# Performance work log

Hardware: AMD Instinct MI355X
Metric: run time of the kernel (lower is better)

The kernel has to match this reference:

```python
import jax, jax.numpy as jnp
import numpy as np

K_EXPERTS = 2  # init kwarg k_experts

def _glu_mlp(x, up_w, gate_w, down_w):
    # gated MLP: down( up(x) * GELU(gate(x)) ), exact-erf GELU matching torch nn.GELU()
    h = (x @ up_w) * jax.nn.gelu(x @ gate_w, approximate=False)
    return h @ down_w

def setup_inputs() -> dict:
    key = jax.random.key(0)
    ks = jax.random.split(key, 8)
    B, S, D, I, E = 2, 2048, 1024, 512, 8
    sc = 0.02
    return {
        "x": jax.random.normal(ks[0], (B, S, D), jnp.float32),
        "gate_w": jax.random.normal(ks[1], (E, D), jnp.float32) * sc,
        "up_w": jax.random.normal(ks[2], (E, D, I), jnp.float32) * sc,
        "gproj_w": jax.random.normal(ks[3], (E, D, I), jnp.float32) * sc,
        "down_w": jax.random.normal(ks[4], (E, I, D), jnp.float32) * sc,
        "shared_up_w": jax.random.normal(ks[5], (D, I), jnp.float32) * sc,
        "shared_gate_w": jax.random.normal(ks[6], (D, I), jnp.float32) * sc,
        "shared_down_w": jax.random.normal(ks[7], (I, D), jnp.float32) * sc,
    }

def reference(x, gate_w, up_w, gproj_w, down_w, shared_up_w, shared_gate_w, shared_down_w):
    B, S, D = x.shape
    E = gate_w.shape[0]
    xf = x.reshape(-1, D)                      # [T, D]
    T = xf.shape[0]

    # --- SigmaGate: softmax over expert logits, top-k, renormalize ---
    logits = xf @ gate_w.T                     # [T, E]
    scores = jax.nn.softmax(logits, axis=-1)
    topk_w, topk_idx = jax.lax.top_k(scores, K_EXPERTS)   # [T, k]
    topk_w = topk_w / (topk_w.sum(axis=-1, keepdims=True) + 1e-20)

    # combine weights as dense [T, E] (topk indices are distinct per token)
    combine = jnp.zeros((T, E), xf.dtype).at[jnp.arange(T)[:, None], topk_idx].add(topk_w)

    # --- experts: scan over E, accumulate weighted expert outputs ---
    def step(acc, ws):
        uw, gw, dw, ce = ws                    # ce: [T] combine weight for this expert
        y_e = _glu_mlp(xf, uw, gw, dw)         # [T, D]
        return acc + ce[:, None] * y_e, None

    y, _ = jax.lax.scan(step, jnp.zeros_like(xf), (up_w, gproj_w, down_w, combine.T))

    # --- shared expert on identity ---
    y = y + _glu_mlp(xf, shared_up_w, shared_gate_w, shared_down_w)
    return y.reshape(B, S, D)
```

## Files before the change

### kernel.cpp

```cpp
#include <hip/hip_runtime.h>
#include <hip/hip_bf16.h>
#include <math.h>

#define T_TOK 4096
#define D_DIM 1024
#define I_DIM 512
#define E_EXP 8
#define KSEL 2
#define NPAIR (T_TOK * KSEL)
#define ROUTED_CAP 9216
#define SHARED_BASE ROUTED_CAP
#define RTOT (ROUTED_CAP + T_TOK)
#define MAXTILES 104
#define GRID_G (MAXTILES * 8)

typedef __bf16 bf16x8 __attribute__((ext_vector_type(8)));
typedef float f32x4 __attribute__((ext_vector_type(4)));
typedef unsigned short ushort8 __attribute__((ext_vector_type(8)));

constexpr size_t SZ_XB  = (size_t)T_TOK * D_DIM * 2;
constexpr size_t SZ_UG  = (size_t)E_EXP * 2 * I_DIM * D_DIM * 2;
constexpr size_t SZ_DT  = (size_t)E_EXP * I_DIM * D_DIM * 2;
constexpr size_t SZ_SUG = (size_t)2 * I_DIM * D_DIM * 2;
constexpr size_t SZ_SDT = (size_t)I_DIM * D_DIM * 2;
constexpr size_t SZ_H   = (size_t)RTOT * I_DIM * 2;
constexpr size_t SZ_Y   = (size_t)RTOT * D_DIM * 2;

constexpr size_t OFF_XB   = 0;
constexpr size_t OFF_UG   = OFF_XB  + SZ_XB;
constexpr size_t OFF_DT   = OFF_UG  + SZ_UG;
constexpr size_t OFF_SUG  = OFF_DT  + SZ_DT;
constexpr size_t OFF_SDT  = OFF_SUG + SZ_SUG;
constexpr size_t OFF_H    = OFF_SDT + SZ_SDT;
constexpr size_t OFF_Y    = OFF_H   + SZ_H;
constexpr size_t OFF_TOPKI= OFF_Y   + SZ_Y;
constexpr size_t OFF_TOPKW= OFF_TOPKI + (size_t)NPAIR * 4;
constexpr size_t OFF_INV  = OFF_TOPKW + (size_t)NPAIR * 4;
constexpr size_t OFF_PERM = OFF_INV   + (size_t)NPAIR * 4;
constexpr size_t OFF_META = OFF_PERM  + (size_t)RTOT * 4;

__device__ __forceinline__ unsigned short f2bf(float f) {
  unsigned int u = __float_as_uint(f);
  unsigned int r = (u + 0x7FFFu + ((u >> 16) & 1u)) >> 16;
  return (unsigned short)r;
}
__device__ __forceinline__ float bf2f(unsigned short s) {
  return __uint_as_float(((unsigned int)s) << 16);
}
__device__ __forceinline__ void gload_lds16(const void* g, void* l) {
  __builtin_amdgcn_global_load_lds(
      (const __attribute__((address_space(1))) void*)g,
      (__attribute__((address_space(3))) void*)l, 16, 0, 0);
}

__global__ void transpose_cvt_all(
    const float* __restrict__ upw, const float* __restrict__ gpw,
    const float* __restrict__ dww, const float* __restrict__ sup,
    const float* __restrict__ sgt, const float* __restrict__ sdw,
    unsigned short* __restrict__ UG, unsigned short* __restrict__ sUG,
    unsigned short* __restrict__ Dt, unsigned short* __restrict__ sDt) {
  __shared__ float t[32][33];
  int bid = blockIdx.x;
  const float* in; unsigned short* out;
  int R, C, xt, yt, mode;
  if (bid < 4096)       { int e = bid >> 9, s = bid & 511;
    in = upw + (size_t)e * D_DIM * I_DIM; out = UG + (size_t)e * 2 * I_DIM * D_DIM;
    R = D_DIM; C = I_DIM; xt = s & 15; yt = s >> 4; mode = 0; }
  else if (bid < 8192)  { int b = bid - 4096; int e = b >> 9, s = b & 511;
    in = gpw + (size_t)e * D_DIM * I_DIM; out = UG + (size_t)e * 2 * I_DIM * D_DIM;
    R = D_DIM; C = I_DIM; xt = s & 15; yt = s >> 4; mode = 1; }
  else if (bid < 12288) { int b = bid - 8192; int e = b >> 9, s = b & 511;
    in = dww + (size_t)e * I_DIM * D_DIM; out = Dt + (size_t)e * I_DIM * D_DIM;
    R = I_DIM; C = D_DIM; xt = s & 31; yt = s >> 5; mode = 2; }
  else if (bid < 12800) { int s = bid - 12288;
    in = sup; out = sUG; R = D_DIM; C = I_DIM; xt = s & 15; yt = s >> 4; mode = 0; }
  else if (bid < 13312) { int s = bid - 12800;
    in = sgt; out = sUG; R = D_DIM; C = I_DIM; xt = s & 15; yt = s >> 4; mode = 1; }
  else                  { int s = bid - 13312;
    in = sdw; out = sDt; R = I_DIM; C = D_DIM; xt = s & 31; yt = s >> 5; mode = 2; }
  int c0 = xt * 32, r0 = yt * 32;
  int tx = threadIdx.x, ty = threadIdx.y;
#pragma unroll
  for (int i = 0; i < 4; ++i)
    t[ty + 8 * i][tx] = in[(size_t)(r0 + ty + 8 * i) * C + c0 + tx];
  __syncthreads();
#pragma unroll
  for (int i = 0; i < 4; ++i) {
    int c = c0 + ty + 8 * i;
    int orow = (mode == 2) ? c : (((c >> 4) << 5) + (c & 15) + (mode == 1 ? 16 : 0));
    out[(size_t)orow * R + r0 + tx] = f2bf(t[tx][ty + 8 * i]);
  }
}

__global__ void gating_kernel(const float* __restrict__ x, const float* __restrict__ gw,
                              unsigned short* __restrict__ xb,
                              int* __restrict__ topk_idx, float* __restrict__ topk_w) {
  int lane = threadIdx.x & 63;
  int t = blockIdx.x * 4 + (threadIdx.x >> 6);
  const float4* xr = (const float4*)(x + (size_t)t * D_DIM);
  float4 xv[4];
#pragma unroll
  for (int j = 0; j < 4; ++j) xv[j] = xr[lane + 64 * j];
#pragma unroll
  for (int j = 0; j < 4; ++j) {
    ushort4 o;
    o.x = f2bf(xv[j].x); o.y = f2bf(xv[j].y); o.z = f2bf(xv[j].z); o.w = f2bf(xv[j].w);
    *(ushort4*)&xb[(size_t)t * D_DIM + (lane + 64 * j) * 4] = o;
  }
  float acc[E_EXP];
#pragma unroll
  for (int e = 0; e < E_EXP; ++e) {
    const float4* gr = (const float4*)(gw + (size_t)e * D_DIM);
    float a = 0.f;
#pragma unroll
    for (int j = 0; j < 4; ++j) {
      float4 g = gr[lane + 64 * j];
      a += xv[j].x * g.x + xv[j].y * g.y + xv[j].z * g.z + xv[j].w * g.w;
    }
    acc[e] = a;
  }
#pragma unroll
  for (int off = 32; off; off >>= 1)
#pragma unroll
    for (int e = 0; e < E_EXP; ++e) acc[e] += __shfl_xor(acc[e], off, 64);
  if (lane == 0) {
    int i0 = 0; float m0 = acc[0];
#pragma unroll
    for (int e = 1; e < E_EXP; ++e) if (acc[e] > m0) { m0 = acc[e]; i0 = e; }
    int i1 = -1; float m1 = -1e30f;
#pragma unroll
    for (int e = 0; e < E_EXP; ++e) if (e != i0 && acc[e] > m1) { m1 = acc[e]; i1 = e; }
    float e1 = __expf(m1 - m0);
    float w0 = 1.0f / (1.0f + e1);
    float w1 = e1 / (1.0f + e1);
    topk_idx[2 * t] = i0; topk_idx[2 * t + 1] = i1;
    topk_w[2 * t] = w0;   topk_w[2 * t + 1] = w1;
  }
}

__global__ __launch_bounds__(1024) void route_kernel(
    const int* __restrict__ tidx, int* __restrict__ meta,
    int* __restrict__ perm, int* __restrict__ inv) {
  __shared__ int els[NPAIR];
  __shared__ int cnt_iw[128][E_EXP];
  __shared__ int base_iw[128][E_EXP];
  __shared__ int ebase[E_EXP];
  __shared__ int ecnt[E_EXP];
  int tid = threadIdx.x, lane = tid & 63, wv = tid >> 6;

  for (int it = 0; it < NPAIR / 1024; ++it) {
    int g = it * 1024 + tid;
    int e = tidx[g];
    els[g] = e;
#pragma unroll
    for (int ex = 0; ex < E_EXP; ++ex) {
      unsigned long long m = __ballot(e == ex);
      if (lane == 0) cnt_iw[it * 16 + wv][ex] = __popcll(m);
    }
  }
  __syncthreads();

  if (tid < E_EXP) {
    int s = 0;
    for (int iw = 0; iw < 128; ++iw) { base_iw[iw][tid] = s; s += cnt_iw[iw][tid]; }
    ecnt[tid] = s;
  }
  __syncthreads();

  if (tid == 0) {
    int o = 0, tc = 0;
    int2* m2 = (int2*)meta;
    for (int e = 0; e < E_EXP; ++e) {
      ebase[e] = o;
      int c = ecnt[e];
      int pt = (c + 127) >> 7;
      for (int ti = 0; ti < pt; ++ti) m2[tc++] = make_int2(e, o + ti * 128);
      o += pt * 128;
    }
    for (int ti = 0; ti < T_TOK / 128; ++ti)
      m2[tc++] = make_int2(E_EXP, SHARED_BASE + ti * 128);
    for (; tc < MAXTILES; ++tc) m2[tc] = make_int2(-1, 0);
  }
  __syncthreads();

  for (int it = 0; it < NPAIR / 1024; ++it) {
    int g = it * 1024 + tid;
    int e = els[g];
    int rank = 0;
#pragma unroll
    for (int ex = 0; ex < E_EXP; ++ex) {
      unsigned long long m = __ballot(e == ex);
      if (e == ex) rank = __popcll(m & ((1ull << lane) - 1ull));
    }
    int row = ebase[e] + base_iw[it * 16 + wv][e] + rank;
    perm[row] = g >> 1;
    inv[g] = row;
  }
  {
    int p = tid;
    int e = p >> 7, s = p & 127;
    int c = ecnt[e];
    int padn = (((c + 127) >> 7) << 7) - c;
    if (s < padn) perm[ebase[e] + c + s] = 0;
  }
  for (int t = tid; t < T_TOK; t += 1024) perm[SHARED_BASE + t] = t;
}

__global__ __launch_bounds__(256, 2) void gemm1_kernel(
    const unsigned short* __restrict__ xb, const unsigned short* __restrict__ UG,
    const unsigned short* __restrict__ sUG, unsigned short* __restrict__ H,
    const int* __restrict__ meta, const int* __restrict__ perm) {
  int orig = blockIdx.x;
  int wg = (orig & 7) * (GRID_G / 8) + (orig >> 3);
  int mt = wg >> 3, nt = wg & 7;
  int2 m2 = ((const int2*)meta)[mt];
  int e = m2.x;
  if (e < 0) return;
  int base = m2.y;
  int n0 = nt * 128;
  const unsigned short* B = (e < E_EXP) ? UG + (size_t)e * 2 * I_DIM * D_DIM : sUG;

  __shared__ unsigned short As[2 * 128 * 64];
  __shared__ unsigned short Bs[2 * 128 * 64];

  int tid = threadIdx.x, lane = tid & 63, wv = tid >> 6;
  const unsigned short *gA[4], *gB[4];
  int dL[4];
#pragma unroll
  for (int j = 0; j < 4; ++j) {
    int c = j * 256 + tid;
    int row = c >> 3, q = c & 7, qs = q ^ (row & 7);
    int tok = perm[base + row];
    gA[j] = xb + (size_t)tok * D_DIM + qs * 8;
    gB[j] = B + (size_t)(n0 + row) * D_DIM + qs * 8;
    dL[j] = (j * 256 + wv * 64) * 8;
  }

  f32x4 acc[4][4] = {};
  int wr = (wv >> 1) * 64, wc = (wv & 1) * 64;
  int l15 = lane & 15, l4 = lane >> 4;
  int sx = l15 & 7;

#define STAGE1(buf, k0) do { \
  _Pragma("unroll") \
  for (int j = 0; j < 4; ++j) { \
    gload_lds16(gA[j] + (k0), As + (buf) * 8192 + dL[j]); \
    gload_lds16(gB[j] + (k0), Bs + (buf) * 8192 + dL[j]); \
  } } while (0)

  STAGE1(0, 0);
  const int NK = D_DIM / 64;
  for (int t = 0; t < NK; ++t) {
    int cur = t & 1;
    if (t + 1 < NK) {
      STAGE1(cur ^ 1, (t + 1) * 64);
      asm volatile("s_waitcnt vmcnt(8)" ::: "memory");
    } else {
      asm volatile("s_waitcnt vmcnt(0)" ::: "memory");
    }
    __builtin_amdgcn_s_barrier();
    bf16x8 af[2][4], bfr[2][4];
#pragma unroll
    for (int kh = 0; kh < 2; ++kh) {
      int kb = kh * 4 + l4;
#pragma unroll
      for (int i = 0; i < 4; ++i) {
        af[kh][i]  = *reinterpret_cast<const bf16x8*>(&As[cur * 8192 + (wr + i * 16 + l15) * 64 + (kb ^ sx) * 8]);
        bfr[kh][i] = *reinterpret_cast<const bf16x8*>(&Bs[cur * 8192 + (wc + i * 16 + l15) * 64 + (kb ^ sx) * 8]);
      }
    }
    asm volatile("" ::: "memory");
    __builtin_amdgcn_s_barrier();
    __builtin_amdgcn_s_setprio(1);
#pragma unroll
    for (int kh = 0; kh < 2; ++kh)
#pragma unroll
      for (int i = 0; i < 4; ++i)
#pragma unroll
        for (int j = 0; j < 4; ++j)
          acc[i][j] = __builtin_amdgcn_mfma_f32_16x16x32_bf16(af[kh][i], bfr[kh][j], acc[i][j], 0, 0, 0);
    __builtin_amdgcn_s_setprio(0);
  }
#undef STAGE1

  const float is2 = 0.70710678118654752f;
  int hbase = (n0 >> 1) + (wv & 1) * 32;
#pragma unroll
  for (int i = 0; i < 4; ++i) {
    int row = base + wr + i * 16 + l4 * 4;
#pragma unroll
    for (int m = 0; m < 2; ++m) {
      int col = hbase + m * 16 + l15;
#pragma unroll
      for (int r = 0; r < 4; ++r) {
        float u = acc[i][2 * m][r], g = acc[i][2 * m + 1][r];
        float gl = 0.5f * g * (1.0f + erff(g * is2));
        H[(size_t)(row + r) * I_DIM + col] = f2bf(u * gl);
      }
    }
  }
}

__global__ __launch_bounds__(256, 2) void gemm2_kernel(
    const unsigned short* __restrict__ H, const unsigned short* __restrict__ Dt,
    const unsigned short* __restrict__ sDt, unsigned short* __restrict__ Y,
    const int* __restrict__ meta) {
  int orig = blockIdx.x;
  int wg = (orig & 7) * (GRID_G / 8) + (orig >> 3);
  int mt = wg >> 3, nt = wg & 7;
  int2 m2 = ((const int2*)meta)[mt];
  int e = m2.x;
  if (e < 0) return;
  int base = m2.y;
  int n0 = nt * 128;
  const unsigned short* B = (e < E_EXP) ? Dt + (size_t)e * D_DIM * I_DIM : sDt;

  __shared__ unsigned short As[2 * 128 * 64];
  __shared__ unsigned short Bs[2 * 128 * 64];

  int tid = threadIdx.x, lane = tid & 63, wv = tid >> 6;
  const unsigned short *gA[4], *gB[4];
  int dL[4];
#pragma unroll
  for (int j = 0; j < 4; ++j) {
    int c = j * 256 + tid;
    int row = c >> 3, q = c & 7, qs = q ^ (row & 7);
    gA[j] = H + (size_t)(base + row) * I_DIM + qs * 8;
    gB[j] = B + (size_t)(n0 + row) * I_DIM + qs * 8;
    dL[j] = (j * 256 + wv * 64) * 8;
  }

  f32x4 acc[4][4] = {};
  int wr = (wv >> 1) * 64, wc = (wv & 1) * 64;
  int l15 = lane & 15, l4 = lane >> 4;
  int sx = l15 & 7;

#define STAGE2(buf, k0) do { \
  _Pragma("unroll") \
  for (int j = 0; j < 4; ++j) { \
    gload_lds16(gA[j] + (k0), As + (buf) * 8192 + dL[j]); \
    gload_lds16(gB[j] + (k0), Bs + (buf) * 8192 + dL[j]); \
  } } while (0)

  STAGE2(0, 0);
  const int NK = I_DIM / 64;
  for (int t = 0; t < NK; ++t) {
    int cur = t & 1;
    if (t + 1 < NK) {
      STAGE2(cur ^ 1, (t + 1) * 64);
      asm volatile("s_waitcnt vmcnt(8)" ::: "memory");
    } else {
      asm volatile("s_waitcnt vmcnt(0)" ::: "memory");
    }
    __builtin_amdgcn_s_barrier();
    bf16x8 af[2][4], bfr[2][4];
#pragma unroll
    for (int kh = 0; kh < 2; ++kh) {
      int kb = kh * 4 + l4;
#pragma unroll
      for (int i = 0; i < 4; ++i) {
        af[kh][i]  = *reinterpret_cast<const bf16x8*>(&As[cur * 8192 + (wr + i * 16 + l15) * 64 + (kb ^ sx) * 8]);
        bfr[kh][i] = *reinterpret_cast<const bf16x8*>(&Bs[cur * 8192 + (wc + i * 16 + l15) * 64 + (kb ^ sx) * 8]);
      }
    }
    asm volatile("" ::: "memory");
    __builtin_amdgcn_s_barrier();
    __builtin_amdgcn_s_setprio(1);
#pragma unroll
    for (int kh = 0; kh < 2; ++kh)
#pragma unroll
      for (int i = 0; i < 4; ++i)
#pragma unroll
        for (int j = 0; j < 4; ++j)
          acc[i][j] = __builtin_amdgcn_mfma_f32_16x16x32_bf16(af[kh][i], bfr[kh][j], acc[i][j], 0, 0, 0);
    __builtin_amdgcn_s_setprio(0);
  }
#undef STAGE2

#pragma unroll
  for (int i = 0; i < 4; ++i) {
    int row = base + wr + i * 16 + l4 * 4;
#pragma unroll
    for (int j = 0; j < 4; ++j) {
      int col = n0 + wc + j * 16 + l15;
#pragma unroll
      for (int r = 0; r < 4; ++r)
        Y[(size_t)(row + r) * D_DIM + col] = f2bf(acc[i][j][r]);
    }
  }
}

__global__ void combine_kernel(const unsigned short* __restrict__ Y, const int* __restrict__ inv,
                               const float* __restrict__ tw, float* __restrict__ out) {
  int g = blockIdx.x * 256 + threadIdx.x;
  int t = g >> 7, d0 = (g & 127) * 8;
  int r0 = inv[2 * t], r1 = inv[2 * t + 1];
  float w0 = tw[2 * t], w1 = tw[2 * t + 1];
  ushort8 y0 = *(const ushort8*)&Y[(size_t)r0 * D_DIM + d0];
  ushort8 y1 = *(const ushort8*)&Y[(size_t)r1 * D_DIM + d0];
  ushort8 ys = *(const ushort8*)&Y[(size_t)(SHARED_BASE + t) * D_DIM + d0];
  float o[8];
#pragma unroll
  for (int j = 0; j < 8; ++j)
    o[j] = w0 * bf2f(y0[j]) + w1 * bf2f(y1[j]) + bf2f(ys[j]);
  float4* op = (float4*)(out + (size_t)t * D_DIM + d0);
  op[0] = make_float4(o[0], o[1], o[2], o[3]);
  op[1] = make_float4(o[4], o[5], o[6], o[7]);
}

extern "C" void kernel_launch(void* const* d_in, const int* in_sizes, int n_in,
                              void* d_out, int out_size, void* d_ws, size_t ws_size,
                              hipStream_t stream) {
  const float* x    = (const float*)d_in[0];
  const float* gw   = (const float*)d_in[1];
  const float* upw  = (const float*)d_in[2];
  const float* gpw  = (const float*)d_in[3];
  const float* dww  = (const float*)d_in[4];
  const float* sup  = (const float*)d_in[5];
  const float* sgt  = (const float*)d_in[6];
  const float* sdw  = (const float*)d_in[7];
  float* out = (float*)d_out;

  char* ws = (char*)d_ws;
  unsigned short* xb  = (unsigned short*)(ws + OFF_XB);
  unsigned short* UG  = (unsigned short*)(ws + OFF_UG);
  unsigned short* Dt  = (unsigned short*)(ws + OFF_DT);
  unsigned short* sUG = (unsigned short*)(ws + OFF_SUG);
  unsigned short* sDt = (unsigned short*)(ws + OFF_SDT);
  unsigned short* H   = (unsigned short*)(ws + OFF_H);
  unsigned short* Y   = (unsigned short*)(ws + OFF_Y);
  int*   tki   = (int*)(ws + OFF_TOPKI);
  float* tkw   = (float*)(ws + OFF_TOPKW);
  int*   inv   = (int*)(ws + OFF_INV);
  int*   perm  = (int*)(ws + OFF_PERM);
  int*   meta  = (int*)(ws + OFF_META);

  transpose_cvt_all<<<13824, dim3(32, 8), 0, stream>>>(upw, gpw, dww, sup, sgt, sdw,
                                                       UG, sUG, Dt, sDt);
  gating_kernel<<<T_TOK / 4, 256, 0, stream>>>(x, gw, xb, tki, tkw);
  route_kernel<<<1, 1024, 0, stream>>>(tki, meta, perm, inv);

  gemm1_kernel<<<GRID_G, 256, 0, stream>>>(xb, UG, sUG, H, meta, perm);
  gemm2_kernel<<<GRID_G, 256, 0, stream>>>(H, Dt, sDt, Y, meta);
  combine_kernel<<<(T_TOK * 128) / 256, 256, 0, stream>>>(Y, inv, tkw, out);
}
```

Measured before the change: 110.5 us.

## Enlarge MoE GEMM tiles to 256x256 with 512-thread blocks

Both grouped GEMM kernels move from 128x128 tiles with 4 waves to 256x256 tiles with 8 waves, each wave computing a 128x64 sub-tile. Routing pads expert segments to 256 rows, so the routed capacity and tile metadata change to match. The LDS fragment loads are interleaved per k-half with the MFMAs to keep register pressure in check. Larger tiles raise arithmetic intensity and cut how often weights are re-read. In exchange there are fewer workgroups (224 vs 832) to fill the CUs, more padding rows per expert, double the LDS per block, and higher register use.

```diff
diff --git a/kernel.cpp b/kernel.cpp
--- a/kernel.cpp
+++ b/kernel.cpp
@@ -8,11 +8,11 @@
 #define E_EXP 8
 #define KSEL 2
 #define NPAIR (T_TOK * KSEL)
-#define ROUTED_CAP 9216
+#define ROUTED_CAP 10240
 #define SHARED_BASE ROUTED_CAP
 #define RTOT (ROUTED_CAP + T_TOK)
-#define MAXTILES 104
-#define GRID_G (MAXTILES * 8)
+#define MAXTILES 56
+#define GRID_G (MAXTILES * 4)
 
 typedef __bf16 bf16x8 __attribute__((ext_vector_type(8)));
 typedef float f32x4 __attribute__((ext_vector_type(4)));
@@ -173,12 +173,12 @@
     for (int e = 0; e < E_EXP; ++e) {
       ebase[e] = o;
       int c = ecnt[e];
-      int pt = (c + 127) >> 7;
-      for (int ti = 0; ti < pt; ++ti) m2[tc++] = make_int2(e, o + ti * 128);
-      o += pt * 128;
-    }
-    for (int ti = 0; ti < T_TOK / 128; ++ti)
-      m2[tc++] = make_int2(E_EXP, SHARED_BASE + ti * 128);
+      int pt = (c + 255) >> 8;
+      for (int ti = 0; ti < pt; ++ti) m2[tc++] = make_int2(e, o + ti * 256);
+      o += pt * 256;
+    }
+    for (int ti = 0; ti < T_TOK / 256; ++ti)
+      m2[tc++] = make_int2(E_EXP, SHARED_BASE + ti * 256);
     for (; tc < MAXTILES; ++tc) m2[tc] = make_int2(-1, 0);
   }
   __syncthreads();
@@ -196,56 +196,55 @@
     perm[row] = g >> 1;
     inv[g] = row;
   }
-  {
-    int p = tid;
-    int e = p >> 7, s = p & 127;
+  for (int p = tid; p < E_EXP * 256; p += 1024) {
+    int e = p >> 8, s = p & 255;
     int c = ecnt[e];
-    int padn = (((c + 127) >> 7) << 7) - c;
+    int padn = (((c + 255) >> 8) << 8) - c;
     if (s < padn) perm[ebase[e] + c + s] = 0;
   }
   for (int t = tid; t < T_TOK; t += 1024) perm[SHARED_BASE + t] = t;
 }
 
-__global__ __launch_bounds__(256, 2) void gemm1_kernel(
+__global__ __launch_bounds__(512, 2) void gemm1_kernel(
     const unsigned short* __restrict__ xb, const unsigned short* __restrict__ UG,
     const unsigned short* __restrict__ sUG, unsigned short* __restrict__ H,
     const int* __restrict__ meta, const int* __restrict__ perm) {
   int orig = blockIdx.x;
   int wg = (orig & 7) * (GRID_G / 8) + (orig >> 3);
-  int mt = wg >> 3, nt = wg & 7;
+  int mt = wg >> 2, nt = wg & 3;
   int2 m2 = ((const int2*)meta)[mt];
   int e = m2.x;
   if (e < 0) return;
   int base = m2.y;
-  int n0 = nt * 128;
+  int n0 = nt * 256;
   const unsigned short* B = (e < E_EXP) ? UG + (size_t)e * 2 * I_DIM * D_DIM : sUG;
 
-  __shared__ unsigned short As[2 * 128 * 64];
-  __shared__ unsigned short Bs[2 * 128 * 64];
+  __shared__ unsigned short As[2 * 256 * 64];
+  __shared__ unsigned short Bs[2 * 256 * 64];
 
   int tid = threadIdx.x, lane = tid & 63, wv = tid >> 6;
   const unsigned short *gA[4], *gB[4];
   int dL[4];
 #pragma unroll
   for (int j = 0; j < 4; ++j) {
-    int c = j * 256 + tid;
+    int c = j * 512 + tid;
     int row = c >> 3, q = c & 7, qs = q ^ (row & 7);
     int tok = perm[base + row];
     gA[j] = xb + (size_t)tok * D_DIM + qs * 8;
     gB[j] = B + (size_t)(n0 + row) * D_DIM + qs * 8;
-    dL[j] = (j * 256 + wv * 64) * 8;
-  }
-
-  f32x4 acc[4][4] = {};
-  int wr = (wv >> 1) * 64, wc = (wv & 1) * 64;
+    dL[j] = (j * 512 + wv * 64) * 8;
+  }
+
+  f32x4 acc[8][4] = {};
+  int wr = (wv >> 2) * 128, wc = (wv & 3) * 64;
   int l15 = lane & 15, l4 = lane >> 4;
   int sx = l15 & 7;
 
 #define STAGE1(buf, k0) do { \
   _Pragma("unroll") \
   for (int j = 0; j < 4; ++j) { \
-    gload_lds16(gA[j] + (k0), As + (buf) * 8192 + dL[j]); \
-    gload_lds16(gB[j] + (k0), Bs + (buf) * 8192 + dL[j]); \
+    gload_lds16(gA[j] + (k0), As + (buf) * 16384 + dL[j]); \
+    gload_lds16(gB[j] + (k0), Bs + (buf) * 16384 + dL[j]); \
   } } while (0)
 
   STAGE1(0, 0);
@@ -259,41 +258,40 @@
       asm volatile("s_waitcnt vmcnt(0)" ::: "memory");
     }
     __builtin_amdgcn_s_barrier();
-    bf16x8 af[2][4], bfr[2][4];
 #pragma unroll
     for (int kh = 0; kh < 2; ++kh) {
       int kb = kh * 4 + l4;
-#pragma unroll
-      for (int i = 0; i < 4; ++i) {
-        af[kh][i]  = *reinterpret_cast<const bf16x8*>(&As[cur * 8192 + (wr + i * 16 + l15) * 64 + (kb ^ sx) * 8]);
-        bfr[kh][i] = *reinterpret_cast<const bf16x8*>(&Bs[cur * 8192 + (wc + i * 16 + l15) * 64 + (kb ^ sx) * 8]);
-      }
+      bf16x8 af[8], bfr[4];
+#pragma unroll
+      for (int i = 0; i < 8; ++i)
+        af[i] = *reinterpret_cast<const bf16x8*>(&As[cur * 16384 + (wr + i * 16 + l15) * 64 + (kb ^ sx) * 8]);
+#pragma unroll
+      for (int j = 0; j < 4; ++j)
+        bfr[j] = *reinterpret_cast<const bf16x8*>(&Bs[cur * 16384 + (wc + j * 16 + l15) * 64 + (kb ^ sx) * 8]);
+      __builtin_amdgcn_s_setprio(1);
+#pragma unroll
+      for (int i = 0; i < 8; ++i)
+#pragma unroll
+        for (int j = 0; j < 4; ++j)
+          acc[i][j] = __builtin_amdgcn_mfma_f32_16x16x32_bf16(af[i], bfr[j], acc[i][j], 0, 0, 0);
+      __builtin_amdgcn_s_setprio(0);
     }
     asm volatile("" ::: "memory");
     __builtin_amdgcn_s_barrier();
-    __builtin_amdgcn_s_setprio(1);
-#pragma unroll
-    for (int kh = 0; kh < 2; ++kh)
-#pragma unroll
-      for (int i = 0; i < 4; ++i)
-#pragma unroll
-        for (int j = 0; j < 4; ++j)
-          acc[i][j] = __builtin_amdgcn_mfma_f32_16x16x32_bf16(af[kh][i], bfr[kh][j], acc[i][j], 0, 0, 0);
-    __builtin_amdgcn_s_setprio(0);
   }
 #undef STAGE1
 
   const float is2 = 0.70710678118654752f;
-  int hbase = (n0 >> 1) + (wv & 1) * 32;
-#pragma unroll
-  for (int i = 0; i < 4; ++i) {
+  int cb = ((n0 + wc) >> 1);
+#pragma unroll
+  for (int i = 0; i < 8; ++i) {
     int row = base + wr + i * 16 + l4 * 4;
 #pragma unroll
-    for (int m = 0; m < 2; ++m) {
-      int col = hbase + m * 16 + l15;
+    for (int p = 0; p < 2; ++p) {
+      int col = cb + p * 16 + l15;
 #pragma unroll
       for (int r = 0; r < 4; ++r) {
-        float u = acc[i][2 * m][r], g = acc[i][2 * m + 1][r];
+        float u = acc[i][2 * p][r], g = acc[i][2 * p + 1][r];
         float gl = 0.5f * g * (1.0f + erff(g * is2));
         H[(size_t)(row + r) * I_DIM + col] = f2bf(u * gl);
       }
@@ -301,45 +299,45 @@
   }
 }
 
-__global__ __launch_bounds__(256, 2) void gemm2_kernel(
+__global__ __launch_bounds__(512, 2) void gemm2_kernel(
     const unsigned short* __restrict__ H, const unsigned short* __restrict__ Dt,
     const unsigned short* __restrict__ sDt, unsigned short* __restrict__ Y,
     const int* __restrict__ meta) {
   int orig = blockIdx.x;
   int wg = (orig & 7) * (GRID_G / 8) + (orig >> 3);
-  int mt = wg >> 3, nt = wg & 7;
+  int mt = wg >> 2, nt = wg & 3;
   int2 m2 = ((const int2*)meta)[mt];
   int e = m2.x;
   if (e < 0) return;
   int base = m2.y;
-  int n0 = nt * 128;
+  int n0 = nt * 256;
   const unsigned short* B = (e < E_EXP) ? Dt + (size_t)e * D_DIM * I_DIM : sDt;
 
-  __shared__ unsigned short As[2 * 128 * 64];
-  __shared__ unsigned short Bs[2 * 128 * 64];
+  __shared__ unsigned short As[2 * 256 * 64];
+  __shared__ unsigned short Bs[2 * 256 * 64];
 
   int tid = threadIdx.x, lane = tid & 63, wv = tid >> 6;
   const unsigned short *gA[4], *gB[4];
   int dL[4];
 #pragma unroll
   for (int j = 0; j < 4; ++j) {
-    int c = j * 256 + tid;
+    int c = j * 512 + tid;
     int row = c >> 3, q = c & 7, qs = q ^ (row & 7);
     gA[j] = H + (size_t)(base + row) * I_DIM + qs * 8;
     gB[j] = B + (size_t)(n0 + row) * I_DIM + qs * 8;
-    dL[j] = (j * 256 + wv * 64) * 8;
-  }
-
-  f32x4 acc[4][4] = {};
-  int wr = (wv >> 1) * 64, wc = (wv & 1) * 64;
+    dL[j] = (j * 512 + wv * 64) * 8;
+  }
+
+  f32x4 acc[8][4] = {};
+  int wr = (wv >> 2) * 128, wc = (wv & 3) * 64;
   int l15 = lane & 15, l4 = lane >> 4;
   int sx = l15 & 7;
 
 #define STAGE2(buf, k0) do { \
   _Pragma("unroll") \
   for (int j = 0; j < 4; ++j) { \
-    gload_lds16(gA[j] + (k0), As + (buf) * 8192 + dL[j]); \
-    gload_lds16(gB[j] + (k0), Bs + (buf) * 8192 + dL[j]); \
+    gload_lds16(gA[j] + (k0), As + (buf) * 16384 + dL[j]); \
+    gload_lds16(gB[j] + (k0), Bs + (buf) * 16384 + dL[j]); \
   } } while (0)
 
   STAGE2(0, 0);
@@ -353,32 +351,31 @@
       asm volatile("s_waitcnt vmcnt(0)" ::: "memory");
     }
     __builtin_amdgcn_s_barrier();
-    bf16x8 af[2][4], bfr[2][4];
 #pragma unroll
     for (int kh = 0; kh < 2; ++kh) {
       int kb = kh * 4 + l4;
-#pragma unroll
-      for (int i = 0; i < 4; ++i) {
-        af[kh][i]  = *reinterpret_cast<const bf16x8*>(&As[cur * 8192 + (wr + i * 16 + l15) * 64 + (kb ^ sx) * 8]);
-        bfr[kh][i] = *reinterpret_cast<const bf16x8*>(&Bs[cur * 8192 + (wc + i * 16 + l15) * 64 + (kb ^ sx) * 8]);
-      }
+      bf16x8 af[8], bfr[4];
+#pragma unroll
+      for (int i = 0; i < 8; ++i)
+        af[i] = *reinterpret_cast<const bf16x8*>(&As[cur * 16384 + (wr + i * 16 + l15) * 64 + (kb ^ sx) * 8]);
+#pragma unroll
+      for (int j = 0; j < 4; ++j)
+        bfr[j] = *reinterpret_cast<const bf16x8*>(&Bs[cur * 16384 + (wc + j * 16 + l15) * 64 + (kb ^ sx) * 8]);
+      __builtin_amdgcn_s_setprio(1);
+#pragma unroll
+      for (int i = 0; i < 8; ++i)
+#pragma unroll
+        for (int j = 0; j < 4; ++j)
+          acc[i][j] = __builtin_amdgcn_mfma_f32_16x16x32_bf16(af[i], bfr[j], acc[i][j], 0, 0, 0);
+      __builtin_amdgcn_s_setprio(0);
     }
     asm volatile("" ::: "memory");
     __builtin_amdgcn_s_barrier();
-    __builtin_amdgcn_s_setprio(1);
-#pragma unroll
-    for (int kh = 0; kh < 2; ++kh)
-#pragma unroll
-      for (int i = 0; i < 4; ++i)
-#pragma unroll
-        for (int j = 0; j < 4; ++j)
-          acc[i][j] = __builtin_amdgcn_mfma_f32_16x16x32_bf16(af[kh][i], bfr[kh][j], acc[i][j], 0, 0, 0);
-    __builtin_amdgcn_s_setprio(0);
   }
 #undef STAGE2
 
 #pragma unroll
-  for (int i = 0; i < 4; ++i) {
+  for (int i = 0; i < 8; ++i) {
     int row = base + wr + i * 16 + l4 * 4;
 #pragma unroll
     for (int j = 0; j < 4; ++j) {
@@ -440,7 +437,7 @@
   gating_kernel<<<T_TOK / 4, 256, 0, stream>>>(x, gw, xb, tki, tkw);
   route_kernel<<<1, 1024, 0, stream>>>(tki, meta, perm, inv);
 
-  gemm1_kernel<<<GRID_G, 256, 0, stream>>>(xb, UG, sUG, H, meta, perm);
-  gemm2_kernel<<<GRID_G, 256, 0, stream>>>(H, Dt, sDt, Y, meta);
+  gemm1_kernel<<<GRID_G, 512, 0, stream>>>(xb, UG, sUG, H, meta, perm);
+  gemm2_kernel<<<GRID_G, 512, 0, stream>>>(H, Dt, sDt, Y, meta);
   combine_kernel<<<(T_TOK * 128) / 256, 256, 0, stream>>>(Y, inv, tkw, out);
 }
```

After: 110.6 us. Within noise of the previous version (+0.1%).
